# Performance work log

Measured on AMD Instinct MI355X. Metric: run time of the kernel, lower is better.

The kernel has to match this reference:

```python
import jax, jax.numpy as jnp
import numpy as np

LN_EPS = 1e-5


def setup_inputs() -> dict:
    key = jax.random.key(0)
    ks = jax.random.split(key, 14)
    b, T, C = 1, 1024, 192
    ATTN, CONT, F = 4, 2, 8  # attn_dims, content_dims, conv feature channels
    s = 0.05
    H = jax.random.normal(ks[0], (b, C, T), jnp.float32)
    d = jax.random.randint(ks[1], (b, T), 2, 8)            # durations in [2,8)
    src_mask = jnp.ones((b, 1, T), dtype=bool)             # True = valid token
    return {
        "H": H, "d": d, "src_mask": src_mask,
        # proj_in: Linear(C,C) + SiLU
        "W_in": jax.random.normal(ks[2], (C, C)) * s, "b_in": jnp.zeros((C,)),
        # ConvLN: Conv1d(C->8, k=3, pad=1) + LayerNorm(8)
        "conv_w": jax.random.normal(ks[3], (F, C, 3)) * s, "conv_b": jnp.zeros((F,)),
        "gamma": jnp.ones((F,)), "beta": jnp.zeros((F,)),
        # W_proj: Linear(10,10)+SiLU+Linear(10,4)+softmax(dim=t_text)
        "wp1": jax.random.normal(ks[4], (10, 10)) * s, "bp1": jnp.zeros((10,)),
        "wp2": jax.random.normal(ks[5], (10, ATTN)) * s, "bp2": jnp.zeros((ATTN,)),
        # C_proj: Linear(10,10)+SiLU+Linear(10,2)+SiLU
        "wc1": jax.random.normal(ks[6], (10, 10)) * s, "bc1": jnp.zeros((10,)),
        "wc2": jax.random.normal(ks[7], (10, CONT)) * s, "bc2": jnp.zeros((CONT,)),
        # proj_WH: Linear(4*C, C); proj_WC: Linear(4*2, C)
        "W_WH": jax.random.normal(ks[8], (ATTN * C, C)) * s, "b_WH": jnp.zeros((C,)),
        "W_WC": jax.random.normal(ks[9], (ATTN * CONT, C)) * s, "b_WC": jnp.zeros((C,)),
        # proj_out: Conv1d(C, C, 1) == pointwise linear over channels
        "W_out": jax.random.normal(ks[10], (C, C)) * s, "b_out": jnp.zeros((C,)),
    }


def reference(H, d, src_mask, W_in, b_in, conv_w, conv_b, gamma, beta,
              wp1, bp1, wp2, bp2, wc1, bc1, wc2, bc2,
              W_WH, b_WH, W_WC, b_WC, W_out, b_out):
    b, C, T = H.shape
    df = d.astype(jnp.float32)
    mel_len = jnp.sum(d, axis=1)                                  # [b]
    t_mel = int(jnp.max(mel_len))                                 # static from concrete d
    frame_valid = jnp.arange(t_mel)[None, :] < mel_len[:, None]   # [b,M] True=valid frame
    tbm = (src_mask[:, 0, None, :] & frame_valid[:, :, None]).astype(jnp.float32)  # [b,M,T]

    # token boundary grid: S = frame_idx - start, E = end - frame_idx
    i = jnp.arange(1, t_mel + 1, dtype=jnp.float32)[None, :, None]  # [1,M,1]
    E_d = jnp.cumsum(df, axis=1)[:, None, :]                        # [b,1,T] token ends
    S_d = E_d - df[:, None, :]                                      # [b,1,T] token starts
    S = (i - S_d) * tbm                                             # [b,M,T]
    E = (E_d - i) * tbm                                             # [b,M,T]

    # proj_in (on [b,T,C]) then ConvLN(C->8) + SiLU
    x = jax.nn.silu(jnp.einsum('bct,cd->btd', H, W_in) + b_in)      # [b,T,C]
    xc = jax.lax.conv_general_dilated(
        jnp.transpose(x, (0, 2, 1)), conv_w, (1,), [(1, 1)],
        dimension_numbers=('NCH', 'OIH', 'NCH')) + conv_b[None, :, None]  # [b,8,T]
    xt = jnp.transpose(xc, (0, 2, 1))                               # [b,T,8]
    mu = jnp.mean(xt, axis=-1, keepdims=True)
    var = jnp.mean(jnp.square(xt - mu), axis=-1, keepdims=True)
    xt = (xt - mu) * jax.lax.rsqrt(var + LN_EPS) * gamma + beta
    xf = jax.nn.silu(xt)                                            # [b,T,8]

    # broadcast conv features over mel frames, cat with S/E boundary scalars
    feats = jnp.concatenate(
        [S[..., None], E[..., None],
         jnp.broadcast_to(xf[:, None, :, :], (b, t_mel, T, xf.shape[-1]))],
        axis=-1)                                                    # [b,M,T,10]

    # W_proj: tiny MLP + softmax over t_text
    W_att = jax.nn.softmax(jax.nn.silu(feats @ wp1 + bp1) @ wp2 + bp2, axis=2)  # [b,M,T,4]
    # C_proj: tiny MLP with SiLU output
    Cm = jax.nn.silu(jax.nn.silu(feats @ wc1 + bc1) @ wc2 + bc2)    # [b,M,T,2]

    WC = jnp.einsum('bmtq,bmtp->bmqp', W_att, Cm).reshape(b, t_mel, -1)  # [b,M,8]
    WH = jnp.einsum('bmtq,bht->bmqh', W_att, H).reshape(b, t_mel, -1)    # [b,M,768]
    O = (WC @ W_WC + b_WC) + (WH @ W_WH + b_WH)                     # [b,M,C]
    O = O @ W_out + b_out                                           # proj_out (1x1 conv)
    O = jnp.transpose(O, (0, 2, 1)) * frame_valid[:, None, :].astype(O.dtype)  # [b,C,M]
    return O, ~frame_valid
```

## Files before the change

kernel.cpp:

```cpp
#include <hip/hip_runtime.h>
#include <math.h>

#define T 1024
#define C 192
#define LN_EPS 1e-5f

typedef __attribute__((ext_vector_type(4))) float f32x4;
typedef __attribute__((ext_vector_type(8))) __bf16 bf16x8;

__device__ __forceinline__ float silu_f(float x){
    return x * __builtin_amdgcn_rcpf(1.0f + __expf(-x));
}
__device__ __forceinline__ float wred_max(float v){
    #pragma unroll
    for(int o=32;o;o>>=1) v = fmaxf(v, __shfl_xor(v,o));
    return v;
}

__global__ void k_scan(const int* __restrict__ d, float* __restrict__ Sd, float* __restrict__ Ed){
    __shared__ int s[T];
    int tid = threadIdx.x;
    int v = d[tid];
    s[tid] = v;
    for(int off=1; off<T; off<<=1){
        __syncthreads();
        int add = (tid>=off) ? s[tid-off] : 0;
        __syncthreads();
        s[tid] += add;
    }
    __syncthreads();
    Ed[tid] = (float)s[tid];
    Sd[tid] = (float)(s[tid]-v);
}

__global__ void k_proj_in(const float* __restrict__ H, const float* __restrict__ W_in,
                          const float* __restrict__ b_in, float* __restrict__ x){
    __shared__ float Hs[192*4];
    int tid = threadIdx.x;
    int t0 = blockIdx.x*4;
    for(int idx=tid; idx<768; idx+=192){
        int ci = idx>>2, j = idx&3;
        Hs[idx] = H[ci*T + t0 + j];
    }
    __syncthreads();
    int c = tid;
    float acc[4];
    float bb = b_in[c];
    #pragma unroll
    for(int j=0;j<4;j++) acc[j] = bb;
    for(int ci=0; ci<192; ci++){
        float wv = W_in[ci*C + c];
        float4 h4 = *(const float4*)&Hs[ci*4];
        acc[0] += h4.x*wv; acc[1] += h4.y*wv;
        acc[2] += h4.z*wv; acc[3] += h4.w*wv;
    }
    #pragma unroll
    for(int j=0;j<4;j++) x[(t0+j)*C + c] = silu_f(acc[j]);
}

__global__ void k_conv_ln(const float* __restrict__ x, const float* __restrict__ conv_w,
                          const float* __restrict__ conv_b, const float* __restrict__ gamma,
                          const float* __restrict__ beta, float* __restrict__ xf){
    __shared__ float part[16][8][2];
    __shared__ float xcv[16][8];
    int tid = threadIdx.x;
    int cc = tid & 1, f = (tid>>1)&7, tl = tid>>4;
    int t = blockIdx.x*16 + tl;
    float acc = 0.f;
    for(int k=0;k<3;k++){
        int tt = t + k - 1;
        if(tt>=0 && tt<T){
            const float* xr = x + tt*C + cc*96;
            const float* wr = conv_w + f*C*3 + k + cc*96*3;
            for(int c2=0;c2<96;c2++) acc += xr[c2]*wr[c2*3];
        }
    }
    part[tl][f][cc] = acc;
    __syncthreads();
    if(cc==0){
        xcv[tl][f] = part[tl][f][0] + part[tl][f][1] + conv_b[f];
    }
    __syncthreads();
    if(cc==0){
        float a = xcv[tl][f];
        float mu=0.f;
        #pragma unroll
        for(int j=0;j<8;j++) mu += xcv[tl][j];
        mu *= 0.125f;
        float var=0.f;
        #pragma unroll
        for(int j=0;j<8;j++){ float dd = xcv[tl][j]-mu; var += dd*dd; }
        var *= 0.125f;
        float vi = rsqrtf(var + LN_EPS);
        float v = (a - mu)*vi*gamma[f] + beta[f];
        xf[t*8+f] = silu_f(v);
    }
}

__global__ void k_A(const float* __restrict__ Sd, const float* __restrict__ Ed,
                    const float* __restrict__ xf,
                    const float* __restrict__ wp1, const float* __restrict__ bp1,
                    const float* __restrict__ wc1, const float* __restrict__ bc1,
                    float* __restrict__ A1, float* __restrict__ A2, float* __restrict__ uv){
    int b = blockIdx.x, tid = threadIdx.x;
    if(b==4){
        if(tid<10){
            uv[tid]    = wp1[tid] - wp1[10+tid];
            uv[10+tid] = wc1[tid] - wc1[10+tid];
        }
        return;
    }
    int t = b*256 + tid;
    float sd = Sd[t], ed = Ed[t];
    float xv[8];
    #pragma unroll
    for(int k=0;k<8;k++) xv[k] = xf[t*8+k];
    #pragma unroll
    for(int j=0;j<10;j++){
        float a1 = bp1[j] - sd*wp1[j] + ed*wp1[10+j];
        float a2 = bc1[j] - sd*wc1[j] + ed*wc1[10+j];
        #pragma unroll
        for(int k=0;k<8;k++){
            a1 += xv[k]*wp1[(2+k)*10+j];
            a2 += xv[k]*wc1[(2+k)*10+j];
        }
        A1[t*12+j] = a1;
        A2[t*12+j] = a2;
    }
    A1[t*12+10]=0.f; A1[t*12+11]=0.f;
    A2[t*12+10]=0.f; A2[t*12+11]=0.f;
}

__global__ void k_prep(const float* __restrict__ W_WH, const float* __restrict__ W_WC,
                       const float* __restrict__ b_WH, const float* __restrict__ b_WC,
                       const float* __restrict__ W_out, const float* __restrict__ b_out,
                       const float* __restrict__ H,
                       __bf16* __restrict__ WfT, float* __restrict__ b2,
                       __bf16* __restrict__ Hb){
    int bid = blockIdx.x, tid = threadIdx.x;
    if(bid >= 778){
        int base = ((bid-778)*256 + tid)*8;
        float4 a = *(const float4*)(H + base);
        float4 b = *(const float4*)(H + base + 4);
        bf16x8 o;
        o[0]=(__bf16)a.x; o[1]=(__bf16)a.y; o[2]=(__bf16)a.z; o[3]=(__bf16)a.w;
        o[4]=(__bf16)b.x; o[5]=(__bf16)b.y; o[6]=(__bf16)b.z; o[7]=(__bf16)b.w;
        *(bf16x8*)(Hb + base) = o;
        return;
    }
    int i = bid, c = tid;
    if(c >= 192) return;
    if(i < 768){
        float a = 0.f;
        for(int j=0;j<C;j++) a += W_WH[i*C+j]*W_out[j*C+c];
        WfT[c*800 + i] = (__bf16)a;
    } else if(i < 776){
        int r = i-768;
        float a = 0.f;
        for(int j=0;j<C;j++) a += W_WC[r*C+j]*W_out[j*C+c];
        WfT[c*800 + 768 + r] = (__bf16)a;
    } else if(i == 776){
        float a = b_out[c];
        for(int j=0;j<C;j++) a += (b_WH[j]+b_WC[j])*W_out[j*C+c];
        b2[c] = a;
    } else {
        for(int k=c; k<192*24; k+=192){
            int cc = k/24, j = k - (k/24)*24;
            WfT[cc*800 + 776 + j] = (__bf16)0.f;
        }
    }
}

__global__ void __launch_bounds__(256) __attribute__((amdgpu_waves_per_eu(4,4)))
k_main(const __bf16* __restrict__ Hb, const float* __restrict__ A1, const float* __restrict__ A2,
       const float* __restrict__ uv,
       const float* __restrict__ wp2, const float* __restrict__ bp2,
       const float* __restrict__ wc2, const float* __restrict__ bc2,
       const __bf16* __restrict__ WfT, const float* __restrict__ b2g,
       __bf16* __restrict__ Eg,
       float* __restrict__ out, int M)
{
    __shared__ __align__(16) __bf16 PTlb[4*832];
    __shared__ __align__(16) __bf16 clds[9*1024];
    __shared__ float scr[64];
    __shared__ float wsm[96];

    int tid = threadIdx.x;
    int w = tid >> 6, lane = tid & 63;
    int m0 = blockIdx.x*4;
    __bf16* Eblk = Eg + (size_t)m0*4096;

    if(tid < 40)      wsm[tid] = wp2[tid];
    else if(tid < 44) wsm[tid] = bp2[tid-40];
    else if(tid < 64) wsm[tid] = wc2[tid-44];
    else if(tid < 66) wsm[tid] = bc2[tid-64];
    else if(tid < 86) wsm[tid] = uv[tid-66];
    if(tid < 224){
        int fb = tid/56, k = 776 + (tid - (tid/56)*56);
        PTlb[fb*832 + (k ^ (fb<<3))] = (__bf16)0.f;
    }
    for(int i=tid;i<1024;i+=256) clds[8*1024 + i] = (__bf16)1.0f;
    __syncthreads();

    for(int mi=0; mi<4; mi++){
        float fi = (float)(m0 + 1 + mi);
        float l[4][4];
        #pragma unroll 1
        for(int tt=0; tt<4; tt++){
            int t = tid*4 + tt;
            float4 a0 = *(const float4*)(A1 + t*12);
            float4 a1 = *(const float4*)(A1 + t*12 + 4);
            float4 a2v = *(const float4*)(A1 + t*12 + 8);
            float Av[10] = {a0.x,a0.y,a0.z,a0.w,a1.x,a1.y,a1.z,a1.w,a2v.x,a2v.y};
            float l0=wsm[40], l1=wsm[41], l2=wsm[42], l3=wsm[43];
            #pragma unroll
            for(int j=0;j<10;j++){
                float h = silu_f(Av[j] + fi*wsm[66+j]);
                l0 += h*wsm[j*4+0]; l1 += h*wsm[j*4+1];
                l2 += h*wsm[j*4+2]; l3 += h*wsm[j*4+3];
            }
            l[tt][0]=l0; l[tt][1]=l1; l[tt][2]=l2; l[tt][3]=l3;
        }
        #pragma unroll
        for(int q=0;q<4;q++){
            float lm = fmaxf(fmaxf(l[0][q],l[1][q]), fmaxf(l[2][q],l[3][q]));
            lm = wred_max(lm);
            if(lane==0) scr[mi*16 + w*4 + q] = lm;
        }

        __bf16 c0v[4], c1v[4];
        #pragma unroll 1
        for(int tt=0; tt<4; tt++){
            int t = tid*4 + tt;
            float4 b0 = *(const float4*)(A2 + t*12);
            float4 b1 = *(const float4*)(A2 + t*12 + 4);
            float4 b2v = *(const float4*)(A2 + t*12 + 8);
            float Bv[10] = {b0.x,b0.y,b0.z,b0.w,b1.x,b1.y,b1.z,b1.w,b2v.x,b2v.y};
            float g1c0 = wsm[64], g1c1 = wsm[65];
            #pragma unroll
            for(int j=0;j<10;j++){
                float g = silu_f(Bv[j] + fi*wsm[76+j]);
                g1c0 += g*wsm[44 + j*2 + 0];
                g1c1 += g*wsm[44 + j*2 + 1];
            }
            c0v[tt] = (__bf16)silu_f(g1c0);
            c1v[tt] = (__bf16)silu_f(g1c1);
        }
        {
            int r0 = mi*2, r1 = mi*2+1;
            int e0 = (tid*4) ^ ((r0&7)<<3);
            int e1 = (tid*4) ^ ((r1&7)<<3);
            *(uint2*)&clds[r0*1024 + e0] = *(uint2*)c0v;
            *(uint2*)&clds[r1*1024 + e1] = *(uint2*)c1v;
        }
        __syncthreads();

        float mxq[4];
        #pragma unroll
        for(int q=0;q<4;q++){
            float a = fmaxf(scr[mi*16+0*4+q], scr[mi*16+1*4+q]);
            float b = fmaxf(scr[mi*16+2*4+q], scr[mi*16+3*4+q]);
            mxq[q] = fmaxf(a,b);
        }
        __bf16* Erow = Eblk + mi*4096;
        #pragma unroll
        for(int q=0;q<4;q++){
            __bf16 ev[4];
            #pragma unroll
            for(int tt=0;tt<4;tt++) ev[tt] = (__bf16)__expf(l[tt][q] - mxq[q]);
            *(uint2*)&Erow[q*1024 + tid*4] = *(uint2*)ev;
        }
    }
    __syncthreads();

    int cl = lane & 15, kg = lane >> 4;
    f32x4 acc1[3];
    f32x4 cw = (f32x4){0.f,0.f,0.f,0.f};
    #pragma unroll
    for(int i=0;i<3;i++) acc1[i] = (f32x4){0.f,0.f,0.f,0.f};
    const __bf16* Aptr = Hb + (size_t)(w*48 + cl)*1024 + kg*8;
    const __bf16* Bp   = Eblk + cl*1024 + kg*8;
    int arow = (cl < 9) ? cl : 8;
    const __bf16* Cp   = clds + arow*1024;
    int swzC = (arow&7)<<3;
    #pragma unroll 2
    for(int ks=0; ks<32; ks++){
        int k0 = ks*32;
        bf16x8 bf = *(const bf16x8*)(Bp + k0);
        bf16x8 cf = *(const bf16x8*)&Cp[(k0 + kg*8) ^ swzC];
        cw = __builtin_amdgcn_mfma_f32_16x16x32_bf16(cf, bf, cw, 0, 0, 0);
        #pragma unroll
        for(int i=0;i<3;i++){
            bf16x8 af = *(const bf16x8*)(Aptr + i*16*1024 + k0);
            acc1[i] = __builtin_amdgcn_mfma_f32_16x16x32_bf16(af, bf, acc1[i], 0, 0, 0);
        }
    }
    float spv  = __shfl(cw[0], 32 + cl);
    float invv = 1.0f / spv;

    {
        int mi_c = cl >> 2, q2 = cl & 3;
        if(w == 3 && kg == (mi_c >> 1)){
            float a0, a1;
            if(mi_c & 1){ a0 = cw[2]; a1 = cw[3]; }
            else        { a0 = cw[0]; a1 = cw[1]; }
            int base = mi_c*832, swzf = mi_c<<3;
            PTlb[base + ((768 + q2*2 + 0) ^ swzf)] = (__bf16)(a0*invv);
            PTlb[base + ((768 + q2*2 + 1) ^ swzf)] = (__bf16)(a1*invv);
        }
    }
    {
        int fb = cl >> 2, qP = cl & 3;
        int swz = fb<<3;
        #pragma unroll
        for(int i=0;i<3;i++){
            int hb = w*48 + i*16 + kg*4;
            #pragma unroll
            for(int r=0;r<4;r++){
                int k = qP*192 + hb + r;
                PTlb[fb*832 + (k ^ swz)] = (__bf16)(acc1[i][r] * invv);
            }
        }
    }
    __syncthreads();

    f32x4 acc2[3];
    #pragma unroll
    for(int i=0;i<3;i++) acc2[i] = (f32x4){0.f,0.f,0.f,0.f};
    const __bf16* A2p = WfT + (size_t)(w*48 + cl)*800 + kg*8;
    int prow = (cl&3)*832, swz2 = (cl&3)<<3;
    #pragma unroll 2
    for(int ks=0; ks<25; ks++){
        int k0 = ks*32;
        bf16x8 bb = *(const bf16x8*)&PTlb[prow + ((k0 + kg*8) ^ swz2)];
        #pragma unroll
        for(int i=0;i<3;i++){
            bf16x8 af = *(const bf16x8*)(A2p + i*16*800 + k0);
            acc2[i] = __builtin_amdgcn_mfma_f32_16x16x32_bf16(af, bb, acc2[i], 0, 0, 0);
        }
    }
    if(cl < 4 && m0 + cl < M){
        #pragma unroll
        for(int i=0;i<3;i++){
            int cb = w*48 + i*16 + kg*4;
            #pragma unroll
            for(int r=0;r<4;r++){
                out[(size_t)(cb+r)*M + m0 + cl] = acc2[i][r] + b2g[cb+r];
            }
        }
    }
    if(tid < 4 && m0 + tid < M) out[(size_t)C*M + m0 + tid] = 0.f;
}

extern "C" void kernel_launch(void* const* d_in, const int* in_sizes, int n_in,
                              void* d_out, int out_size, void* d_ws, size_t ws_size,
                              hipStream_t stream)
{
    const float* H      = (const float*)d_in[0];
    const int*   d      = (const int*)  d_in[1];
    const float* W_in   = (const float*)d_in[3];
    const float* b_in   = (const float*)d_in[4];
    const float* conv_w = (const float*)d_in[5];
    const float* conv_b = (const float*)d_in[6];
    const float* gamma  = (const float*)d_in[7];
    const float* beta   = (const float*)d_in[8];
    const float* wp1    = (const float*)d_in[9];
    const float* bp1    = (const float*)d_in[10];
    const float* wp2    = (const float*)d_in[11];
    const float* bp2    = (const float*)d_in[12];
    const float* wc1    = (const float*)d_in[13];
    const float* bc1    = (const float*)d_in[14];
    const float* wc2    = (const float*)d_in[15];
    const float* bc2    = (const float*)d_in[16];
    const float* W_WH   = (const float*)d_in[17];
    const float* b_WH   = (const float*)d_in[18];
    const float* W_WC   = (const float*)d_in[19];
    const float* b_WC   = (const float*)d_in[20];
    const float* W_out  = (const float*)d_in[21];
    const float* b_out  = (const float*)d_in[22];

    float* out = (float*)d_out;
    int M = out_size / 193;

    float* ws   = (float*)d_ws;
    float* Sd   = ws;
    float* Ed   = ws + 1024;
    float* A1   = ws + 2048;
    float* A2   = ws + 14336;
    float* uvp  = ws + 26624;
    float* b2   = ws + 26656;
    __bf16* WfT = (__bf16*)(ws + 26848);
    __bf16* Hb  = (__bf16*)(ws + 103648);
    float* x    = ws + 201952;
    float* xf   = ws + 398560;
    __bf16* Eg  = (__bf16*)(ws + 406752);

    hipLaunchKernelGGL(k_scan,    dim3(1),   dim3(1024), 0, stream, d, Sd, Ed);
    hipLaunchKernelGGL(k_prep,    dim3(874), dim3(256),  0, stream,
                       W_WH, W_WC, b_WH, b_WC, W_out, b_out, H, WfT, b2, Hb);
    hipLaunchKernelGGL(k_proj_in, dim3(256), dim3(192),  0, stream, H, W_in, b_in, x);
    hipLaunchKernelGGL(k_conv_ln, dim3(64),  dim3(256),  0, stream, x, conv_w, conv_b, gamma, beta, xf);
    hipLaunchKernelGGL(k_A,       dim3(5),   dim3(256),  0, stream, Sd, Ed, xf, wp1, bp1, wc1, bc1, A1, A2, uvp);
    hipLaunchKernelGGL(k_main,    dim3((M+3)/4), dim3(256), 0, stream,
                       Hb, A1, A2, uvp, wp2, bp2, wc2, bc2, WfT, b2, Eg, out, M);
}
```

Measured before the change: 221.6 us.

## Assign one mel frame per wave and reduce softmax and content sums in registers

The prologue now gives each wave one mel frame instead of having the whole block loop over four frames with a block barrier per frame. Each wave finds the per-query max in a first pass over tokens. A second pass recomputes the logits, writes the exponentials and accumulates the softmax denominators and the content-weighted sums with wave shuffles. This drops the LDS content buffer, the extra MFMA that computed sums and content contractions, and several barriers. The cost is computing the logits MLP twice and issuing narrower scalar stores of the exponentials.

Result: slower. 237.0 us (+6.9%).

```diff
diff --git a/kernel.cpp b/kernel.cpp
--- a/kernel.cpp
+++ b/kernel.cpp
@@ -14,6 +14,11 @@
 __device__ __forceinline__ float wred_max(float v){
     #pragma unroll
     for(int o=32;o;o>>=1) v = fmaxf(v, __shfl_xor(v,o));
+    return v;
+}
+__device__ __forceinline__ float wred_sum(float v){
+    #pragma unroll
+    for(int o=32;o;o>>=1) v += __shfl_xor(v,o);
     return v;
 }
 
@@ -181,7 +186,6 @@
        float* __restrict__ out, int M)
 {
     __shared__ __align__(16) __bf16 PTlb[4*832];
-    __shared__ __align__(16) __bf16 clds[9*1024];
     __shared__ float scr[64];
     __shared__ float wsm[96];
 
@@ -195,122 +199,114 @@
     else if(tid < 64) wsm[tid] = wc2[tid-44];
     else if(tid < 66) wsm[tid] = bc2[tid-64];
     else if(tid < 86) wsm[tid] = uv[tid-66];
-    if(tid < 224){
-        int fb = tid/56, k = 776 + (tid - (tid/56)*56);
+    if(tid >= 128 && tid < 128+224){
+        int j = tid - 128;
+        int fb = j/56, k = 776 + (j - (j/56)*56);
         PTlb[fb*832 + (k ^ (fb<<3))] = (__bf16)0.f;
     }
-    for(int i=tid;i<1024;i+=256) clds[8*1024 + i] = (__bf16)1.0f;
-    __syncthreads();
-
-    for(int mi=0; mi<4; mi++){
-        float fi = (float)(m0 + 1 + mi);
-        float l[4][4];
-        #pragma unroll 1
-        for(int tt=0; tt<4; tt++){
-            int t = tid*4 + tt;
-            float4 a0 = *(const float4*)(A1 + t*12);
-            float4 a1 = *(const float4*)(A1 + t*12 + 4);
-            float4 a2v = *(const float4*)(A1 + t*12 + 8);
-            float Av[10] = {a0.x,a0.y,a0.z,a0.w,a1.x,a1.y,a1.z,a1.w,a2v.x,a2v.y};
-            float l0=wsm[40], l1=wsm[41], l2=wsm[42], l3=wsm[43];
-            #pragma unroll
-            for(int j=0;j<10;j++){
-                float h = silu_f(Av[j] + fi*wsm[66+j]);
-                l0 += h*wsm[j*4+0]; l1 += h*wsm[j*4+1];
-                l2 += h*wsm[j*4+2]; l3 += h*wsm[j*4+3];
-            }
-            l[tt][0]=l0; l[tt][1]=l1; l[tt][2]=l2; l[tt][3]=l3;
-        }
-        #pragma unroll
-        for(int q=0;q<4;q++){
-            float lm = fmaxf(fmaxf(l[0][q],l[1][q]), fmaxf(l[2][q],l[3][q]));
-            lm = wred_max(lm);
-            if(lane==0) scr[mi*16 + w*4 + q] = lm;
-        }
-
-        __bf16 c0v[4], c1v[4];
-        #pragma unroll 1
-        for(int tt=0; tt<4; tt++){
-            int t = tid*4 + tt;
-            float4 b0 = *(const float4*)(A2 + t*12);
-            float4 b1 = *(const float4*)(A2 + t*12 + 4);
-            float4 b2v = *(const float4*)(A2 + t*12 + 8);
-            float Bv[10] = {b0.x,b0.y,b0.z,b0.w,b1.x,b1.y,b1.z,b1.w,b2v.x,b2v.y};
-            float g1c0 = wsm[64], g1c1 = wsm[65];
-            #pragma unroll
-            for(int j=0;j<10;j++){
-                float g = silu_f(Bv[j] + fi*wsm[76+j]);
-                g1c0 += g*wsm[44 + j*2 + 0];
-                g1c1 += g*wsm[44 + j*2 + 1];
-            }
-            c0v[tt] = (__bf16)silu_f(g1c0);
-            c1v[tt] = (__bf16)silu_f(g1c1);
-        }
-        {
-            int r0 = mi*2, r1 = mi*2+1;
-            int e0 = (tid*4) ^ ((r0&7)<<3);
-            int e1 = (tid*4) ^ ((r1&7)<<3);
-            *(uint2*)&clds[r0*1024 + e0] = *(uint2*)c0v;
-            *(uint2*)&clds[r1*1024 + e1] = *(uint2*)c1v;
-        }
-        __syncthreads();
-
-        float mxq[4];
-        #pragma unroll
-        for(int q=0;q<4;q++){
-            float a = fmaxf(scr[mi*16+0*4+q], scr[mi*16+1*4+q]);
-            float b = fmaxf(scr[mi*16+2*4+q], scr[mi*16+3*4+q]);
-            mxq[q] = fmaxf(a,b);
-        }
-        __bf16* Erow = Eblk + mi*4096;
-        #pragma unroll
-        for(int q=0;q<4;q++){
-            __bf16 ev[4];
-            #pragma unroll
-            for(int tt=0;tt<4;tt++) ev[tt] = (__bf16)__expf(l[tt][q] - mxq[q]);
-            *(uint2*)&Erow[q*1024 + tid*4] = *(uint2*)ev;
-        }
+    __syncthreads();
+
+    float fi = (float)(m0 + 1 + w);
+
+    float pmax4[4] = {-3.0e38f,-3.0e38f,-3.0e38f,-3.0e38f};
+    #pragma unroll 1
+    for(int ch=0; ch<16; ch++){
+        int t = ch*64 + lane;
+        float4 a0 = *(const float4*)(A1 + t*12);
+        float4 a1 = *(const float4*)(A1 + t*12 + 4);
+        float4 a2v = *(const float4*)(A1 + t*12 + 8);
+        float Av[10] = {a0.x,a0.y,a0.z,a0.w,a1.x,a1.y,a1.z,a1.w,a2v.x,a2v.y};
+        float l0=wsm[40], l1=wsm[41], l2=wsm[42], l3=wsm[43];
+        #pragma unroll
+        for(int j=0;j<10;j++){
+            float h = silu_f(Av[j] + fi*wsm[66+j]);
+            l0 += h*wsm[j*4+0]; l1 += h*wsm[j*4+1];
+            l2 += h*wsm[j*4+2]; l3 += h*wsm[j*4+3];
+        }
+        pmax4[0]=fmaxf(pmax4[0],l0); pmax4[1]=fmaxf(pmax4[1],l1);
+        pmax4[2]=fmaxf(pmax4[2],l2); pmax4[3]=fmaxf(pmax4[3],l3);
+    }
+    #pragma unroll
+    for(int q=0;q<4;q++) pmax4[q] = wred_max(pmax4[q]);
+
+    float sp4[4] = {0.f,0.f,0.f,0.f};
+    float wcp2[4][2];
+    #pragma unroll
+    for(int q=0;q<4;q++){ wcp2[q][0]=0.f; wcp2[q][1]=0.f; }
+    __bf16* Erow = Eblk + w*4096;
+    #pragma unroll 1
+    for(int ch=0; ch<16; ch++){
+        int t = ch*64 + lane;
+        float4 a0 = *(const float4*)(A1 + t*12);
+        float4 a1 = *(const float4*)(A1 + t*12 + 4);
+        float4 a2v = *(const float4*)(A1 + t*12 + 8);
+        float Av[10] = {a0.x,a0.y,a0.z,a0.w,a1.x,a1.y,a1.z,a1.w,a2v.x,a2v.y};
+        float l0=wsm[40], l1=wsm[41], l2=wsm[42], l3=wsm[43];
+        #pragma unroll
+        for(int j=0;j<10;j++){
+            float h = silu_f(Av[j] + fi*wsm[66+j]);
+            l0 += h*wsm[j*4+0]; l1 += h*wsm[j*4+1];
+            l2 += h*wsm[j*4+2]; l3 += h*wsm[j*4+3];
+        }
+        float e0 = __expf(l0 - pmax4[0]);
+        float e1 = __expf(l1 - pmax4[1]);
+        float e2 = __expf(l2 - pmax4[2]);
+        float e3 = __expf(l3 - pmax4[3]);
+        Erow[0*1024 + t] = (__bf16)e0;
+        Erow[1*1024 + t] = (__bf16)e1;
+        Erow[2*1024 + t] = (__bf16)e2;
+        Erow[3*1024 + t] = (__bf16)e3;
+        sp4[0]+=e0; sp4[1]+=e1; sp4[2]+=e2; sp4[3]+=e3;
+
+        float4 b0 = *(const float4*)(A2 + t*12);
+        float4 b1 = *(const float4*)(A2 + t*12 + 4);
+        float4 b2v = *(const float4*)(A2 + t*12 + 8);
+        float Bv[10] = {b0.x,b0.y,b0.z,b0.w,b1.x,b1.y,b1.z,b1.w,b2v.x,b2v.y};
+        float g1c0 = wsm[64], g1c1 = wsm[65];
+        #pragma unroll
+        for(int j=0;j<10;j++){
+            float g = silu_f(Bv[j] + fi*wsm[76+j]);
+            g1c0 += g*wsm[44 + j*2 + 0];
+            g1c1 += g*wsm[44 + j*2 + 1];
+        }
+        float c0 = silu_f(g1c0), c1 = silu_f(g1c1);
+        wcp2[0][0]+=e0*c0; wcp2[0][1]+=e0*c1;
+        wcp2[1][0]+=e1*c0; wcp2[1][1]+=e1*c1;
+        wcp2[2][0]+=e2*c0; wcp2[2][1]+=e2*c1;
+        wcp2[3][0]+=e3*c0; wcp2[3][1]+=e3*c1;
+    }
+    #pragma unroll
+    for(int q=0;q<4;q++){
+        sp4[q] = wred_sum(sp4[q]);
+        wcp2[q][0] = wred_sum(wcp2[q][0]);
+        wcp2[q][1] = wred_sum(wcp2[q][1]);
+    }
+    if(lane < 4) scr[w*4 + lane] = 1.0f / sp4[lane];
+    if(lane < 8){
+        int q = lane>>1, p = lane&1;
+        PTlb[w*832 + ((768+lane) ^ (w<<3))] = (__bf16)(wcp2[q][p] / sp4[q]);
     }
     __syncthreads();
 
     int cl = lane & 15, kg = lane >> 4;
     f32x4 acc1[3];
-    f32x4 cw = (f32x4){0.f,0.f,0.f,0.f};
     #pragma unroll
     for(int i=0;i<3;i++) acc1[i] = (f32x4){0.f,0.f,0.f,0.f};
     const __bf16* Aptr = Hb + (size_t)(w*48 + cl)*1024 + kg*8;
     const __bf16* Bp   = Eblk + cl*1024 + kg*8;
-    int arow = (cl < 9) ? cl : 8;
-    const __bf16* Cp   = clds + arow*1024;
-    int swzC = (arow&7)<<3;
     #pragma unroll 2
     for(int ks=0; ks<32; ks++){
         int k0 = ks*32;
         bf16x8 bf = *(const bf16x8*)(Bp + k0);
-        bf16x8 cf = *(const bf16x8*)&Cp[(k0 + kg*8) ^ swzC];
-        cw = __builtin_amdgcn_mfma_f32_16x16x32_bf16(cf, bf, cw, 0, 0, 0);
         #pragma unroll
         for(int i=0;i<3;i++){
             bf16x8 af = *(const bf16x8*)(Aptr + i*16*1024 + k0);
             acc1[i] = __builtin_amdgcn_mfma_f32_16x16x32_bf16(af, bf, acc1[i], 0, 0, 0);
         }
     }
-    float spv  = __shfl(cw[0], 32 + cl);
-    float invv = 1.0f / spv;
-
-    {
-        int mi_c = cl >> 2, q2 = cl & 3;
-        if(w == 3 && kg == (mi_c >> 1)){
-            float a0, a1;
-            if(mi_c & 1){ a0 = cw[2]; a1 = cw[3]; }
-            else        { a0 = cw[0]; a1 = cw[1]; }
-            int base = mi_c*832, swzf = mi_c<<3;
-            PTlb[base + ((768 + q2*2 + 0) ^ swzf)] = (__bf16)(a0*invv);
-            PTlb[base + ((768 + q2*2 + 1) ^ swzf)] = (__bf16)(a1*invv);
-        }
-    }
     {
         int fb = cl >> 2, qP = cl & 3;
+        float invv = scr[cl];
         int swz = fb<<3;
         #pragma unroll
         for(int i=0;i<3;i++){
```
